# Kernel tuning notes

Hardware: AMD Instinct MI355X
Metric: run time of the kernel (lower is better)

The kernel has to match this reference:

```python
import jax, jax.numpy as jnp
import numpy as np

FEATURE_DIM = 128
HIDDEN_DIM = 64
MAPPING_SIZE = 64
SCALE = 10.0
B, N, H, W = 8, 65536, 56, 56


def setup_inputs() -> dict:
    key = jax.random.key(0)
    ks = jax.random.split(key, 12)
    features = jax.random.normal(ks[0], (B, FEATURE_DIM, H, W), dtype=jnp.float32)
    # points in [-1, 1]^3
    points = jax.random.uniform(ks[1], (B, N, 3), dtype=jnp.float32, minval=-1.0, maxval=1.0)
    # realistic pinhole intrinsics for a 56x56 feature map
    k_mat = jnp.array([[56.0, 0.0, 28.0], [0.0, 56.0, 28.0], [0.0, 0.0, 1.0]], dtype=jnp.float32)
    k = jnp.broadcast_to(k_mat, (B, 3, 3))
    # extrinsics: identity rotation, translate z by 2 so points are in front of camera
    rt_mat = jnp.concatenate([jnp.eye(3, dtype=jnp.float32), jnp.array([[0.0], [0.0], [2.0]], dtype=jnp.float32)], axis=1)
    rt = jnp.broadcast_to(rt_mat, (B, 3, 4))
    # learned params
    B_gauss = jax.random.normal(ks[2], (MAPPING_SIZE, 3), dtype=jnp.float32) * SCALE
    input_dim = FEATURE_DIM + 2 * MAPPING_SIZE
    W1 = jax.random.normal(ks[3], (input_dim, HIDDEN_DIM), dtype=jnp.float32) * 0.05
    b1 = jnp.zeros((HIDDEN_DIM,), dtype=jnp.float32)
    W2 = jax.random.normal(ks[4], (HIDDEN_DIM, HIDDEN_DIM), dtype=jnp.float32) * 0.05
    b2 = jnp.zeros((HIDDEN_DIM,), dtype=jnp.float32)
    W3 = jax.random.normal(ks[5], (HIDDEN_DIM, HIDDEN_DIM), dtype=jnp.float32) * 0.05
    b3 = jnp.zeros((HIDDEN_DIM,), dtype=jnp.float32)
    W4 = jax.random.normal(ks[6], (HIDDEN_DIM, 1), dtype=jnp.float32) * 0.05
    b4 = jnp.zeros((1,), dtype=jnp.float32)
    return {"features": features, "points": points, "k": k, "rt": rt,
            "B_gauss": B_gauss, "W1": W1, "b1": b1, "W2": W2, "b2": b2,
            "W3": W3, "b3": b3, "W4": W4, "b4": b4}


def _grid_sample_bilinear_zeros(grid, x, y):
    # grid: (B, C, H, W); x, y: (B, N) pixel coords (align_corners=False already unnormalized)
    Bc, C, Hc, Wc = grid.shape
    g = jnp.transpose(grid, (0, 2, 3, 1))  # (B, H, W, C)
    x0 = jnp.floor(x)
    y0 = jnp.floor(y)
    wx1 = x - x0  # frac
    wy1 = y - y0
    wx0 = 1.0 - wx1
    wy0 = 1.0 - wy1
    x0i = x0.astype(jnp.int32)
    y0i = y0.astype(jnp.int32)
    bidx = jnp.arange(Bc, dtype=jnp.int32)[:, None]  # (B, 1)

    def gather(ix, iy):
        inb = ((ix >= 0) & (ix < Wc) & (iy >= 0) & (iy < Hc)).astype(grid.dtype)  # (B, N)
        vals = g[bidx, jnp.clip(iy, 0, Hc - 1), jnp.clip(ix, 0, Wc - 1)]  # (B, N, C)
        return vals * inb[..., None]

    out = (gather(x0i, y0i) * (wx0 * wy0)[..., None]
           + gather(x0i + 1, y0i) * (wx1 * wy0)[..., None]
           + gather(x0i, y0i + 1) * (wx0 * wy1)[..., None]
           + gather(x0i + 1, y0i + 1) * (wx1 * wy1)[..., None])
    return out  # (B, N, C)


def reference(features, points, k, rt, B_gauss, W1, b1, W2, b2, W3, b3, W4, b4):
    Bc, Nc, _ = points.shape
    Hc, Wc = features.shape[-2:]
    # --- camera projection ---
    homo = jnp.concatenate([points, jnp.ones((Bc, Nc, 1), dtype=points.dtype)], axis=2)  # (B,N,4)
    cam = jnp.einsum('bij,bnj->bni', rt, homo)   # (B,N,3)
    img = jnp.einsum('bij,bnj->bni', k, cam)     # (B,N,3)
    z = img[:, :, 2:3] + 1e-8
    uv = img[:, :, :2] / z
    valid = (img[:, :, 2:3] > 0).astype(points.dtype)  # (B,N,1)
    u_norm = (2.0 * uv[..., 0] + 1.0) / Wc - 1.0
    v_norm = (2.0 * uv[..., 1] + 1.0) / Hc - 1.0
    # grid_sample align_corners=False unnormalization: ix = ((g+1)*W - 1)/2
    x = ((u_norm + 1.0) * Wc - 1.0) * 0.5
    y = ((v_norm + 1.0) * Hc - 1.0) * 0.5
    img_feats = _grid_sample_bilinear_zeros(features, x, y) * valid  # (B,N,C)
    # --- Fourier mapping ---
    x_proj = (2.0 * np.pi) * jnp.einsum('bnd,md->bnm', points, B_gauss)  # (B,N,M)
    coord_feats = jnp.concatenate([jnp.sin(x_proj), jnp.cos(x_proj)], axis=-1)  # (B,N,2M)
    # --- MLP ---
    inp = jnp.concatenate([img_feats, coord_feats], axis=2)  # (B,N,C+2M)
    h = jax.nn.relu(inp @ W1 + b1)
    h = jax.nn.relu(h @ W2 + b2)
    h = jax.nn.relu(h @ W3 + b3)
    out = h @ W4 + b4  # (B,N,1)
    return out
```

## Files before the change

kernel.cpp:

```cpp
#include <hip/hip_runtime.h>

#define FDIM 128
#define HDIM 64
#define MSIZE 64
#define IMG_W 56
#define IMG_H 56
#define NPIX (IMG_W * IMG_H)
#define NB 8
#define NPTS 65536

typedef _Float16 f16x8 __attribute__((ext_vector_type(8)));
typedef __fp16 hf16x2 __attribute__((ext_vector_type(2)));
typedef float f32x4 __attribute__((ext_vector_type(4)));
typedef int i32x4 __attribute__((ext_vector_type(4)));

#define W2_OFF 16384
#define W3_OFF 20480
#define FT_BYTE_OFF 49152
#define TR16_BLOCKS (NPIX / 16 * NB)

__device__ __forceinline__ void lds_fence() {
    __asm__ volatile("s_waitcnt lgkmcnt(0)" ::: "memory");
}

__global__ __launch_bounds__(256) void prep_kernel(const float* __restrict__ in,
                                                   const float* __restrict__ W1,
                                                   const float* __restrict__ W2,
                                                   const float* __restrict__ W3,
                                                   _Float16* __restrict__ ws) {
    if (blockIdx.x < TR16_BLOCKS) {
        __shared__ float tile[16][133];
        _Float16* out = ws + FT_BYTE_OFF / 2;
        const int b = blockIdx.x / (NPIX / 16);
        const int pbase = (blockIdx.x % (NPIX / 16)) * 16;
        const int t = threadIdx.x;
        const float* src = in + (size_t)b * FDIM * NPIX;
        _Float16*    dst = out + (size_t)b * NPIX * FDIM;
        const int pq = t & 3;
        const int ch = t >> 2;
#pragma unroll
        for (int it = 0; it < 2; ++it) {
            const int c = it * 64 + ch;
            const float4 v = *(const float4*)(src + (size_t)c * NPIX + pbase + pq * 4);
            tile[pq * 4 + 0][c] = v.x;
            tile[pq * 4 + 1][c] = v.y;
            tile[pq * 4 + 2][c] = v.z;
            tile[pq * 4 + 3][c] = v.w;
        }
        __syncthreads();
        const int px = t >> 4;
        const int hk = (t & 15) * 8;
        union { f16x8 v; hf16x2 h[4]; } hv;
#pragma unroll
        for (int j = 0; j < 4; ++j)
            hv.h[j] = __builtin_amdgcn_cvt_pkrtz(tile[px][hk + 2 * j], tile[px][hk + 2 * j + 1]);
        *(f16x8*)(dst + (size_t)(pbase + px) * FDIM + hk) = hv.v;
    } else {
        const int t = (blockIdx.x - TR16_BLOCKS) * 256 + threadIdx.x;
        const int l = t & 63;
        const int q = l >> 4;
        const int col = l & 15;
        const int frag = t >> 6;
        if (frag < 32) {
            const int kt = frag >> 2, nt = frag & 3;
#pragma unroll
            for (int j = 0; j < 8; ++j) {
                int k = kt * 32 + q * 8 + j;
                int row = (k < 128) ? k : (128 + (k & 1) * 64 + ((k - 128) >> 1));
                ws[((size_t)(frag * 64 + l)) * 8 + j] = (_Float16)W1[row * HDIM + nt * 16 + col];
            }
        } else if (frag < 40) {
            const int f2 = frag - 32;
            const int kt = f2 >> 2, nt = f2 & 3;
#pragma unroll
            for (int j = 0; j < 8; ++j) {
                int row = kt * 32 + q * 8 + j;
                ws[W2_OFF + ((size_t)(f2 * 64 + l)) * 8 + j] = (_Float16)W2[row * HDIM + nt * 16 + col];
            }
        } else {
            const int f3 = frag - 40;
            const int kt = f3 >> 2, nt = f3 & 3;
#pragma unroll
            for (int j = 0; j < 8; ++j) {
                int row = kt * 32 + q * 8 + j;
                ws[W3_OFF + ((size_t)(f3 * 64 + l)) * 8 + j] = (_Float16)W3[row * HDIM + nt * 16 + col];
            }
        }
    }
}

__global__ __launch_bounds__(256, 4) void decoder_mfma3(
    const _Float16* __restrict__ ft,
    const float* __restrict__ points,
    const float* __restrict__ Kmat, const float* __restrict__ Rt,
    const float* __restrict__ Bg,
    const _Float16* __restrict__ wfrag,
    const float* __restrict__ b1, const float* __restrict__ b2,
    const float* __restrict__ b3,
    const float* __restrict__ W4, const float* __restrict__ b4,
    float* __restrict__ out) {
    __shared__ _Float16 lds[4 * 32 * 72];
    const int tid = threadIdx.x;
    const int wid = tid >> 6;
    const int l   = tid & 63;
    const int q   = l >> 4;
    const int col = l & 15;
    const int b    = blockIdx.x & 7;
    const int grp  = blockIdx.x >> 3;
    const int base = b * NPTS + grp * 128 + wid * 32;
    _Float16* Ah = lds + wid * 32 * 72;
    float* sh = (float*)Ah;
    int*   shi = (int*)Ah;

    if (l < 32) {
        const int gid = base + l;
        const float px = points[(size_t)gid * 3 + 0];
        const float py = points[(size_t)gid * 3 + 1];
        const float pz = points[(size_t)gid * 3 + 2];
        const float* rt = Rt + b * 12;
        const float* km = Kmat + b * 9;
        float cx = rt[0] * px + rt[1] * py + rt[2]  * pz + rt[3];
        float cy = rt[4] * px + rt[5] * py + rt[6]  * pz + rt[7];
        float cz = rt[8] * px + rt[9] * py + rt[10] * pz + rt[11];
        float ix = km[0] * cx + km[1] * cy + km[2] * cz;
        float iy = km[3] * cx + km[4] * cy + km[5] * cz;
        float iz = km[6] * cx + km[7] * cy + km[8] * cz;
        float z  = iz + 1e-8f;
        float u  = ix / z;
        float v  = iy / z;
        float valid = (iz > 0.0f) ? 1.0f : 0.0f;
        float u_norm = (2.0f * u + 1.0f) / (float)IMG_W - 1.0f;
        float v_norm = (2.0f * v + 1.0f) / (float)IMG_H - 1.0f;
        float x = ((u_norm + 1.0f) * (float)IMG_W - 1.0f) * 0.5f;
        float y = ((v_norm + 1.0f) * (float)IMG_H - 1.0f) * 0.5f;
        float x0f = floorf(x), y0f = floorf(y);
        float wx1 = x - x0f, wy1 = y - y0f;
        float wx0 = 1.0f - wx1, wy0 = 1.0f - wy1;
        int x0 = (int)x0f, y0 = (int)y0f;
        int x1 = x0 + 1, y1 = y0 + 1;
        int x0c = x0 < 0 ? 0 : (x0 > IMG_W - 1 ? IMG_W - 1 : x0);
        int x1c = x1 < 0 ? 0 : (x1 > IMG_W - 1 ? IMG_W - 1 : x1);
        int y0c = y0 < 0 ? 0 : (y0 > IMG_H - 1 ? IMG_H - 1 : y0);
        int y1c = y1 < 0 ? 0 : (y1 > IMG_H - 1 ? IMG_H - 1 : y1);
        float mx0 = (x0 >= 0 && x0 < IMG_W) ? 1.0f : 0.0f;
        float mx1 = (x1 >= 0 && x1 < IMG_W) ? 1.0f : 0.0f;
        float my0 = (y0 >= 0 && y0 < IMG_H) ? 1.0f : 0.0f;
        float my1 = (y1 >= 0 && y1 < IMG_H) ? 1.0f : 0.0f;
        const int pb = b * NPIX;
        sh[l * 12 + 0] = wx0 * wy0 * mx0 * my0 * valid;
        sh[l * 12 + 1] = wx1 * wy0 * mx1 * my0 * valid;
        sh[l * 12 + 2] = wx0 * wy1 * mx0 * my1 * valid;
        sh[l * 12 + 3] = wx1 * wy1 * mx1 * my1 * valid;
        shi[l * 12 + 4] = (pb + y0c * IMG_W + x0c) * FDIM;
        shi[l * 12 + 5] = (pb + y0c * IMG_W + x1c) * FDIM;
        shi[l * 12 + 6] = (pb + y1c * IMG_W + x0c) * FDIM;
        shi[l * 12 + 7] = (pb + y1c * IMG_W + x1c) * FDIM;
        sh[l * 12 + 8]  = px;
        sh[l * 12 + 9]  = py;
        sh[l * 12 + 10] = pz;
    }
    lds_fence();

    const f32x4 zero4 = {0.0f, 0.0f, 0.0f, 0.0f};
    f32x4 acc[2][4];
#pragma unroll
    for (int mt = 0; mt < 2; ++mt)
#pragma unroll
        for (int nt = 0; nt < 4; ++nt) acc[mt][nt] = zero4;

    f32x4 wv[2];
    i32x4 iv[2];
    float qx[2], qy[2], qz[2];
#pragma unroll
    for (int mt = 0; mt < 2; ++mt) {
        const float* e = sh + (mt * 16 + col) * 12;
        wv[mt] = *(const f32x4*)(e);
        iv[mt] = *(const i32x4*)(e + 4);
        qx[mt] = e[8]; qy[mt] = e[9]; qz[mt] = e[10];
    }

    f16x8 c00 = *(const f16x8*)(ft + iv[0].x + q * 8);
    f16x8 c10 = *(const f16x8*)(ft + iv[0].y + q * 8);
    f16x8 c01 = *(const f16x8*)(ft + iv[0].z + q * 8);
    f16x8 c11 = *(const f16x8*)(ft + iv[0].w + q * 8);

#pragma unroll
    for (int ktf = 0; ktf < 4; ++ktf) {
        float bgx[4], bgy[4], bgz[4];
#pragma unroll
        for (int i = 0; i < 4; ++i) {
            const int m = ktf * 16 + q * 4 + i;
            bgx[i] = Bg[m * 3 + 0];
            bgy[i] = Bg[m * 3 + 1];
            bgz[i] = Bg[m * 3 + 2];
        }
        f16x8 bf[4];
#pragma unroll
        for (int nt = 0; nt < 4; ++nt)
            bf[nt] = *(const f16x8*)(wfrag + ((size_t)(((4 + ktf) * 4 + nt) * 64 + l)) * 8);
#pragma unroll
        for (int mt = 0; mt < 2; ++mt) {
            union { f16x8 v; hf16x2 h[4]; } af;
#pragma unroll
            for (int i = 0; i < 4; ++i) {
                float t = bgx[i] * qx[mt] + bgy[i] * qy[mt] + bgz[i] * qz[mt];
                float tf = __builtin_amdgcn_fractf(t);
                af.h[i] = __builtin_amdgcn_cvt_pkrtz(__builtin_amdgcn_sinf(tf),
                                                     __builtin_amdgcn_cosf(tf));
            }
#pragma unroll
            for (int nt = 0; nt < 4; ++nt)
                acc[mt][nt] = __builtin_amdgcn_mfma_f32_16x16x32_f16(af.v, bf[nt], acc[mt][nt], 0, 0, 0);
        }
    }

    _Float16 wh[2][4];
#pragma unroll
    for (int mt = 0; mt < 2; ++mt) {
        wh[mt][0] = (_Float16)wv[mt].x; wh[mt][1] = (_Float16)wv[mt].y;
        wh[mt][2] = (_Float16)wv[mt].z; wh[mt][3] = (_Float16)wv[mt].w;
    }
#pragma unroll
    for (int s = 0; s < 8; ++s) {
        const int mt = s >> 2, ktg = s & 3;
        f16x8 n00, n10, n01, n11;
        if (s < 7) {
            const int nmt = (s + 1) >> 2, nktg = (s + 1) & 3;
            const int co = nktg * 32 + q * 8;
            n00 = *(const f16x8*)(ft + iv[nmt].x + co);
            n10 = *(const f16x8*)(ft + iv[nmt].y + co);
            n01 = *(const f16x8*)(ft + iv[nmt].z + co);
            n11 = *(const f16x8*)(ft + iv[nmt].w + co);
        }
        f16x8 af = c00 * wh[mt][0] + c10 * wh[mt][1] + c01 * wh[mt][2] + c11 * wh[mt][3];
#pragma unroll
        for (int nt = 0; nt < 4; ++nt) {
            f16x8 bf = *(const f16x8*)(wfrag + ((size_t)((ktg * 4 + nt) * 64 + l)) * 8);
            acc[mt][nt] = __builtin_amdgcn_mfma_f32_16x16x32_f16(af, bf, acc[mt][nt], 0, 0, 0);
        }
        c00 = n00; c10 = n10; c01 = n01; c11 = n11;
    }

    float bb[4];
#pragma unroll
    for (int nt = 0; nt < 4; ++nt) bb[nt] = b1[nt * 16 + col];
#pragma unroll
    for (int mt = 0; mt < 2; ++mt)
#pragma unroll
        for (int nt = 0; nt < 4; ++nt)
#pragma unroll
            for (int r = 0; r < 4; ++r) {
                float hv = fmaxf(acc[mt][nt][r] + bb[nt], 0.0f);
                Ah[(mt * 16 + q * 4 + r) * 72 + nt * 16 + col] = (_Float16)hv;
            }
    lds_fence();

#pragma unroll
    for (int mt = 0; mt < 2; ++mt)
#pragma unroll
        for (int nt = 0; nt < 4; ++nt) acc[mt][nt] = zero4;
#pragma unroll
    for (int ktl = 0; ktl < 2; ++ktl) {
        f16x8 bf[4];
#pragma unroll
        for (int nt = 0; nt < 4; ++nt)
            bf[nt] = *(const f16x8*)(wfrag + W2_OFF + ((size_t)((ktl * 4 + nt) * 64 + l)) * 8);
#pragma unroll
        for (int mt = 0; mt < 2; ++mt) {
            f16x8 af = *(const f16x8*)(&Ah[(mt * 16 + col) * 72 + ktl * 32 + q * 8]);
#pragma unroll
            for (int nt = 0; nt < 4; ++nt)
                acc[mt][nt] = __builtin_amdgcn_mfma_f32_16x16x32_f16(af, bf[nt], acc[mt][nt], 0, 0, 0);
        }
    }
    lds_fence();
#pragma unroll
    for (int nt = 0; nt < 4; ++nt) bb[nt] = b2[nt * 16 + col];
#pragma unroll
    for (int mt = 0; mt < 2; ++mt)
#pragma unroll
        for (int nt = 0; nt < 4; ++nt)
#pragma unroll
            for (int r = 0; r < 4; ++r) {
                float hv = fmaxf(acc[mt][nt][r] + bb[nt], 0.0f);
                Ah[(mt * 16 + q * 4 + r) * 72 + nt * 16 + col] = (_Float16)hv;
            }
    lds_fence();

#pragma unroll
    for (int mt = 0; mt < 2; ++mt)
#pragma unroll
        for (int nt = 0; nt < 4; ++nt) acc[mt][nt] = zero4;
#pragma unroll
    for (int ktl = 0; ktl < 2; ++ktl) {
        f16x8 bf[4];
#pragma unroll
        for (int nt = 0; nt < 4; ++nt)
            bf[nt] = *(const f16x8*)(wfrag + W3_OFF + ((size_t)((ktl * 4 + nt) * 64 + l)) * 8);
#pragma unroll
        for (int mt = 0; mt < 2; ++mt) {
            f16x8 af = *(const f16x8*)(&Ah[(mt * 16 + col) * 72 + ktl * 32 + q * 8]);
#pragma unroll
            for (int nt = 0; nt < 4; ++nt)
                acc[mt][nt] = __builtin_amdgcn_mfma_f32_16x16x32_f16(af, bf[nt], acc[mt][nt], 0, 0, 0);
        }
    }

    float b3v[4], w4v[4];
#pragma unroll
    for (int nt = 0; nt < 4; ++nt) {
        b3v[nt] = b3[nt * 16 + col];
        w4v[nt] = W4[nt * 16 + col];
    }
    const float b4v = b4[0];
#pragma unroll
    for (int mt = 0; mt < 2; ++mt)
#pragma unroll
        for (int r = 0; r < 4; ++r) {
            float p = 0.0f;
#pragma unroll
            for (int nt = 0; nt < 4; ++nt)
                p = fmaf(fmaxf(acc[mt][nt][r] + b3v[nt], 0.0f), w4v[nt], p);
            p += __shfl_xor(p, 1);
            p += __shfl_xor(p, 2);
            p += __shfl_xor(p, 4);
            p += __shfl_xor(p, 8);
            if (col == 0) out[base + mt * 16 + q * 4 + r] = p + b4v;
        }
}

__global__ __launch_bounds__(64, 2) void decoder_valu(
    const float* __restrict__ feats, const float* __restrict__ points,
    const float* __restrict__ Kmat, const float* __restrict__ Rt,
    const float* __restrict__ Bg,
    const float* __restrict__ W1, const float* __restrict__ b1,
    const float* __restrict__ W2, const float* __restrict__ b2,
    const float* __restrict__ W3, const float* __restrict__ b3,
    const float* __restrict__ W4, const float* __restrict__ b4,
    float* __restrict__ out) {
    __shared__ float hbuf[64 * 65];
    const int tid = threadIdx.x;
    const int b   = blockIdx.x / (NPTS / 64);
    const int gid = blockIdx.x * 64 + tid;
    const float px = points[(size_t)gid * 3 + 0];
    const float py = points[(size_t)gid * 3 + 1];
    const float pz = points[(size_t)gid * 3 + 2];
    const float* rt = Rt + b * 12;
    const float* km = Kmat + b * 9;
    float cx = rt[0] * px + rt[1] * py + rt[2]  * pz + rt[3];
    float cy = rt[4] * px + rt[5] * py + rt[6]  * pz + rt[7];
    float cz = rt[8] * px + rt[9] * py + rt[10] * pz + rt[11];
    float ix = km[0] * cx + km[1] * cy + km[2] * cz;
    float iy = km[3] * cx + km[4] * cy + km[5] * cz;
    float iz = km[6] * cx + km[7] * cy + km[8] * cz;
    float z  = iz + 1e-8f;
    float u  = ix / z, v = iy / z;
    float valid = (iz > 0.0f) ? 1.0f : 0.0f;
    float u_norm = (2.0f * u + 1.0f) / (float)IMG_W - 1.0f;
    float v_norm = (2.0f * v + 1.0f) / (float)IMG_H - 1.0f;
    float x = ((u_norm + 1.0f) * (float)IMG_W - 1.0f) * 0.5f;
    float y = ((v_norm + 1.0f) * (float)IMG_H - 1.0f) * 0.5f;
    float x0f = floorf(x), y0f = floorf(y);
    float wx1 = x - x0f, wy1 = y - y0f;
    float wx0 = 1.0f - wx1, wy0 = 1.0f - wy1;
    int x0 = (int)x0f, y0 = (int)y0f;
    int x1 = x0 + 1, y1 = y0 + 1;
    int x0c = x0 < 0 ? 0 : (x0 > IMG_W - 1 ? IMG_W - 1 : x0);
    int x1c = x1 < 0 ? 0 : (x1 > IMG_W - 1 ? IMG_W - 1 : x1);
    int y0c = y0 < 0 ? 0 : (y0 > IMG_H - 1 ? IMG_H - 1 : y0);
    int y1c = y1 < 0 ? 0 : (y1 > IMG_H - 1 ? IMG_H - 1 : y1);
    float mx0 = (x0 >= 0 && x0 < IMG_W) ? 1.0f : 0.0f;
    float mx1 = (x1 >= 0 && x1 < IMG_W) ? 1.0f : 0.0f;
    float my0 = (y0 >= 0 && y0 < IMG_H) ? 1.0f : 0.0f;
    float my1 = (y1 >= 0 && y1 < IMG_H) ? 1.0f : 0.0f;
    float w00 = wx0 * wy0 * mx0 * my0 * valid;
    float w10 = wx1 * wy0 * mx1 * my0 * valid;
    float w01 = wx0 * wy1 * mx0 * my1 * valid;
    float w11 = wx1 * wy1 * mx1 * my1 * valid;
    float h[HDIM];
#pragma unroll
    for (int j = 0; j < HDIM; ++j) h[j] = b1[j];
    const float* fb = feats + (size_t)b * FDIM * NPIX;
    const int p00 = y0c * IMG_W + x0c, p10 = y0c * IMG_W + x1c;
    const int p01 = y1c * IMG_W + x0c, p11 = y1c * IMG_W + x1c;
#pragma unroll 1
    for (int c = 0; c < FDIM; ++c) {
        const float* fp = fb + (size_t)c * NPIX;
        float fv = w00 * fp[p00] + w10 * fp[p10] + w01 * fp[p01] + w11 * fp[p11];
        const float* wr = W1 + (size_t)c * HDIM;
#pragma unroll
        for (int j = 0; j < HDIM; ++j) h[j] = fmaf(fv, wr[j], h[j]);
    }
#pragma unroll 1
    for (int m = 0; m < MSIZE; ++m) {
        float t = Bg[m * 3 + 0] * px + Bg[m * 3 + 1] * py + Bg[m * 3 + 2] * pz;
        float tf = t - floorf(t);
        float s = __builtin_amdgcn_sinf(tf);
        float c = __builtin_amdgcn_cosf(tf);
        const float* wsn = W1 + (size_t)(FDIM + m) * HDIM;
        const float* wcs = W1 + (size_t)(FDIM + MSIZE + m) * HDIM;
#pragma unroll
        for (int j = 0; j < HDIM; ++j)
            h[j] = fmaf(s, wsn[j], fmaf(c, wcs[j], h[j]));
    }
    float* myh = &hbuf[tid * 65];
#pragma unroll
    for (int j = 0; j < HDIM; ++j) myh[j] = fmaxf(h[j], 0.0f);
    float h2[HDIM];
#pragma unroll
    for (int j = 0; j < HDIM; ++j) h2[j] = b2[j];
#pragma unroll 1
    for (int i = 0; i < HDIM; ++i) {
        float hi = myh[i];
        const float* wr = W2 + (size_t)i * HDIM;
#pragma unroll
        for (int j = 0; j < HDIM; ++j) h2[j] = fmaf(hi, wr[j], h2[j]);
    }
#pragma unroll
    for (int j = 0; j < HDIM; ++j) myh[j] = fmaxf(h2[j], 0.0f);
#pragma unroll
    for (int j = 0; j < HDIM; ++j) h[j] = b3[j];
#pragma unroll 1
    for (int i = 0; i < HDIM; ++i) {
        float hi = myh[i];
        const float* wr = W3 + (size_t)i * HDIM;
#pragma unroll
        for (int j = 0; j < HDIM; ++j) h[j] = fmaf(hi, wr[j], h[j]);
    }
    float acc = b4[0];
#pragma unroll
    for (int j = 0; j < HDIM; ++j) acc = fmaf(fmaxf(h[j], 0.0f), W4[j], acc);
    out[gid] = acc;
}

extern "C" void kernel_launch(void* const* d_in, const int* in_sizes, int n_in,
                              void* d_out, int out_size, void* d_ws, size_t ws_size,
                              hipStream_t stream) {
    const float* feats = (const float*)d_in[0];
    const float* pts   = (const float*)d_in[1];
    const float* k     = (const float*)d_in[2];
    const float* rt    = (const float*)d_in[3];
    const float* Bg    = (const float*)d_in[4];
    const float* W1    = (const float*)d_in[5];
    const float* b1    = (const float*)d_in[6];
    const float* W2    = (const float*)d_in[7];
    const float* b2    = (const float*)d_in[8];
    const float* W3    = (const float*)d_in[9];
    const float* b3    = (const float*)d_in[10];
    const float* W4    = (const float*)d_in[11];
    const float* b4    = (const float*)d_in[12];
    float* out = (float*)d_out;

    const size_t ftBytes = (size_t)NB * NPIX * FDIM * sizeof(_Float16);

    if (ws_size >= FT_BYTE_OFF + ftBytes) {
        _Float16* wf = (_Float16*)d_ws;
        _Float16* ft = (_Float16*)((char*)d_ws + FT_BYTE_OFF);
        prep_kernel<<<TR16_BLOCKS + 12, 256, 0, stream>>>(feats, W1, W2, W3, wf);
        decoder_mfma3<<<NB * NPTS / 128, 256, 0, stream>>>(ft, pts, k, rt, Bg, wf,
                                                           b1, b2, b3, W4, b4, out);
    } else {
        decoder_valu<<<NB * NPTS / 64, 64, 0, stream>>>(feats, pts, k, rt, Bg,
                                                        W1, b1, W2, b2, W3, b3, W4, b4, out);
    }
}
```

Baseline: 182.3 us.

## Shuffle per-point data in registers and deepen gather prefetch pipeline

Per-point projection results are now computed redundantly by all 64 lanes and distributed with wave shuffles, replacing the LDS staging round trip and fence. The bilinear feature gather prefetch goes from one to two steps ahead, the W2/W3 weight fragments are loaded before the LDS activation write so their latency overlaps it, and the occupancy hint drops from 4 to 3 blocks per CU. This raises register pressure and may reduce occupancy in exchange for more latency hiding on the random gathers.

```diff
diff --git a/kernel.cpp b/kernel.cpp
--- a/kernel.cpp
+++ b/kernel.cpp
@@ -12,7 +12,6 @@
 typedef _Float16 f16x8 __attribute__((ext_vector_type(8)));
 typedef __fp16 hf16x2 __attribute__((ext_vector_type(2)));
 typedef float f32x4 __attribute__((ext_vector_type(4)));
-typedef int i32x4 __attribute__((ext_vector_type(4)));
 
 #define W2_OFF 16384
 #define W3_OFF 20480
@@ -89,7 +88,7 @@
     }
 }
 
-__global__ __launch_bounds__(256, 4) void decoder_mfma3(
+__global__ __launch_bounds__(256, 3) void decoder_mfma4(
     const _Float16* __restrict__ ft,
     const float* __restrict__ points,
     const float* __restrict__ Kmat, const float* __restrict__ Rt,
@@ -109,11 +108,9 @@
     const int grp  = blockIdx.x >> 3;
     const int base = b * NPTS + grp * 128 + wid * 32;
     _Float16* Ah = lds + wid * 32 * 72;
-    float* sh = (float*)Ah;
-    int*   shi = (int*)Ah;
-
-    if (l < 32) {
-        const int gid = base + l;
+
+    {
+        const int gid = base + (l & 31);
         const float px = points[(size_t)gid * 3 + 0];
         const float py = points[(size_t)gid * 3 + 1];
         const float pz = points[(size_t)gid * 3 + 2];
@@ -147,186 +144,198 @@
         float my0 = (y0 >= 0 && y0 < IMG_H) ? 1.0f : 0.0f;
         float my1 = (y1 >= 0 && y1 < IMG_H) ? 1.0f : 0.0f;
         const int pb = b * NPIX;
-        sh[l * 12 + 0] = wx0 * wy0 * mx0 * my0 * valid;
-        sh[l * 12 + 1] = wx1 * wy0 * mx1 * my0 * valid;
-        sh[l * 12 + 2] = wx0 * wy1 * mx0 * my1 * valid;
-        sh[l * 12 + 3] = wx1 * wy1 * mx1 * my1 * valid;
-        shi[l * 12 + 4] = (pb + y0c * IMG_W + x0c) * FDIM;
-        shi[l * 12 + 5] = (pb + y0c * IMG_W + x1c) * FDIM;
-        shi[l * 12 + 6] = (pb + y1c * IMG_W + x0c) * FDIM;
-        shi[l * 12 + 7] = (pb + y1c * IMG_W + x1c) * FDIM;
-        sh[l * 12 + 8]  = px;
-        sh[l * 12 + 9]  = py;
-        sh[l * 12 + 10] = pz;
-    }
-    lds_fence();
-
-    const f32x4 zero4 = {0.0f, 0.0f, 0.0f, 0.0f};
-    f32x4 acc[2][4];
-#pragma unroll
-    for (int mt = 0; mt < 2; ++mt)
-#pragma unroll
-        for (int nt = 0; nt < 4; ++nt) acc[mt][nt] = zero4;
-
-    f32x4 wv[2];
-    i32x4 iv[2];
-    float qx[2], qy[2], qz[2];
-#pragma unroll
-    for (int mt = 0; mt < 2; ++mt) {
-        const float* e = sh + (mt * 16 + col) * 12;
-        wv[mt] = *(const f32x4*)(e);
-        iv[mt] = *(const i32x4*)(e + 4);
-        qx[mt] = e[8]; qy[mt] = e[9]; qz[mt] = e[10];
-    }
-
-    f16x8 c00 = *(const f16x8*)(ft + iv[0].x + q * 8);
-    f16x8 c10 = *(const f16x8*)(ft + iv[0].y + q * 8);
-    f16x8 c01 = *(const f16x8*)(ft + iv[0].z + q * 8);
-    f16x8 c11 = *(const f16x8*)(ft + iv[0].w + q * 8);
-
-#pragma unroll
-    for (int ktf = 0; ktf < 4; ++ktf) {
-        float bgx[4], bgy[4], bgz[4];
-#pragma unroll
-        for (int i = 0; i < 4; ++i) {
-            const int m = ktf * 16 + q * 4 + i;
-            bgx[i] = Bg[m * 3 + 0];
-            bgy[i] = Bg[m * 3 + 1];
-            bgz[i] = Bg[m * 3 + 2];
-        }
-        f16x8 bf[4];
-#pragma unroll
-        for (int nt = 0; nt < 4; ++nt)
-            bf[nt] = *(const f16x8*)(wfrag + ((size_t)(((4 + ktf) * 4 + nt) * 64 + l)) * 8);
+        float r_w00 = wx0 * wy0 * mx0 * my0 * valid;
+        float r_w10 = wx1 * wy0 * mx1 * my0 * valid;
+        float r_w01 = wx0 * wy1 * mx0 * my1 * valid;
+        float r_w11 = wx1 * wy1 * mx1 * my1 * valid;
+        int r_i00 = (pb + y0c * IMG_W + x0c) * FDIM;
+        int r_i10 = (pb + y0c * IMG_W + x1c) * FDIM;
+        int r_i01 = (pb + y1c * IMG_W + x0c) * FDIM;
+        int r_i11 = (pb + y1c * IMG_W + x1c) * FDIM;
+
+        float wv0[2], wv1[2], wv2[2], wv3[2];
+        int   iv0[2], iv1[2], iv2[2], iv3[2];
+        float qx[2], qy[2], qz[2];
 #pragma unroll
         for (int mt = 0; mt < 2; ++mt) {
-            union { f16x8 v; hf16x2 h[4]; } af;
+            const int src = mt * 16 + col;
+            wv0[mt] = __shfl(r_w00, src);
+            wv1[mt] = __shfl(r_w10, src);
+            wv2[mt] = __shfl(r_w01, src);
+            wv3[mt] = __shfl(r_w11, src);
+            iv0[mt] = __shfl(r_i00, src);
+            iv1[mt] = __shfl(r_i10, src);
+            iv2[mt] = __shfl(r_i01, src);
+            iv3[mt] = __shfl(r_i11, src);
+            qx[mt]  = __shfl(px, src);
+            qy[mt]  = __shfl(py, src);
+            qz[mt]  = __shfl(pz, src);
+        }
+
+        const f32x4 zero4 = {0.0f, 0.0f, 0.0f, 0.0f};
+        f32x4 acc[2][4];
+#pragma unroll
+        for (int mt = 0; mt < 2; ++mt)
+#pragma unroll
+            for (int nt = 0; nt < 4; ++nt) acc[mt][nt] = zero4;
+
+        const int co0 = q * 8;
+        f16x8 a00 = *(const f16x8*)(ft + iv0[0] + co0);
+        f16x8 a10 = *(const f16x8*)(ft + iv1[0] + co0);
+        f16x8 a01 = *(const f16x8*)(ft + iv2[0] + co0);
+        f16x8 a11 = *(const f16x8*)(ft + iv3[0] + co0);
+        const int co1 = 32 + q * 8;
+        f16x8 e00 = *(const f16x8*)(ft + iv0[0] + co1);
+        f16x8 e10 = *(const f16x8*)(ft + iv1[0] + co1);
+        f16x8 e01 = *(const f16x8*)(ft + iv2[0] + co1);
+        f16x8 e11 = *(const f16x8*)(ft + iv3[0] + co1);
+
+#pragma unroll
+        for (int ktf = 0; ktf < 4; ++ktf) {
+            float bgx[4], bgy[4], bgz[4];
 #pragma unroll
             for (int i = 0; i < 4; ++i) {
-                float t = bgx[i] * qx[mt] + bgy[i] * qy[mt] + bgz[i] * qz[mt];
-                float tf = __builtin_amdgcn_fractf(t);
-                af.h[i] = __builtin_amdgcn_cvt_pkrtz(__builtin_amdgcn_sinf(tf),
-                                                     __builtin_amdgcn_cosf(tf));
-            }
+                const int m = ktf * 16 + q * 4 + i;
+                bgx[i] = Bg[m * 3 + 0];
+                bgy[i] = Bg[m * 3 + 1];
+                bgz[i] = Bg[m * 3 + 2];
+            }
+            f16x8 bf[4];
 #pragma unroll
             for (int nt = 0; nt < 4; ++nt)
-                acc[mt][nt] = __builtin_amdgcn_mfma_f32_16x16x32_f16(af.v, bf[nt], acc[mt][nt], 0, 0, 0);
-        }
-    }
-
-    _Float16 wh[2][4];
-#pragma unroll
-    for (int mt = 0; mt < 2; ++mt) {
-        wh[mt][0] = (_Float16)wv[mt].x; wh[mt][1] = (_Float16)wv[mt].y;
-        wh[mt][2] = (_Float16)wv[mt].z; wh[mt][3] = (_Float16)wv[mt].w;
-    }
-#pragma unroll
-    for (int s = 0; s < 8; ++s) {
-        const int mt = s >> 2, ktg = s & 3;
-        f16x8 n00, n10, n01, n11;
-        if (s < 7) {
-            const int nmt = (s + 1) >> 2, nktg = (s + 1) & 3;
-            const int co = nktg * 32 + q * 8;
-            n00 = *(const f16x8*)(ft + iv[nmt].x + co);
-            n10 = *(const f16x8*)(ft + iv[nmt].y + co);
-            n01 = *(const f16x8*)(ft + iv[nmt].z + co);
-            n11 = *(const f16x8*)(ft + iv[nmt].w + co);
-        }
-        f16x8 af = c00 * wh[mt][0] + c10 * wh[mt][1] + c01 * wh[mt][2] + c11 * wh[mt][3];
+                bf[nt] = *(const f16x8*)(wfrag + ((size_t)(((4 + ktf) * 4 + nt) * 64 + l)) * 8);
+#pragma unroll
+            for (int mt = 0; mt < 2; ++mt) {
+                union { f16x8 v; hf16x2 h[4]; } af;
+#pragma unroll
+                for (int i = 0; i < 4; ++i) {
+                    float t = bgx[i] * qx[mt] + bgy[i] * qy[mt] + bgz[i] * qz[mt];
+                    float tf = __builtin_amdgcn_fractf(t);
+                    af.h[i] = __builtin_amdgcn_cvt_pkrtz(__builtin_amdgcn_sinf(tf),
+                                                         __builtin_amdgcn_cosf(tf));
+                }
+#pragma unroll
+                for (int nt = 0; nt < 4; ++nt)
+                    acc[mt][nt] = __builtin_amdgcn_mfma_f32_16x16x32_f16(af.v, bf[nt], acc[mt][nt], 0, 0, 0);
+            }
+        }
+
+        _Float16 wh[2][4];
+#pragma unroll
+        for (int mt = 0; mt < 2; ++mt) {
+            wh[mt][0] = (_Float16)wv0[mt]; wh[mt][1] = (_Float16)wv1[mt];
+            wh[mt][2] = (_Float16)wv2[mt]; wh[mt][3] = (_Float16)wv3[mt];
+        }
+#pragma unroll
+        for (int s = 0; s < 8; ++s) {
+            const int mt = s >> 2;
+            f16x8 t00, t10, t01, t11;
+            if (s < 6) {
+                const int nmt = (s + 2) >> 2, nktg = (s + 2) & 3;
+                const int co = nktg * 32 + q * 8;
+                t00 = *(const f16x8*)(ft + iv0[nmt] + co);
+                t10 = *(const f16x8*)(ft + iv1[nmt] + co);
+                t01 = *(const f16x8*)(ft + iv2[nmt] + co);
+                t11 = *(const f16x8*)(ft + iv3[nmt] + co);
+            }
+            f16x8 af = a00 * wh[mt][0] + a10 * wh[mt][1] + a01 * wh[mt][2] + a11 * wh[mt][3];
+            const int ktg = s & 3;
+#pragma unroll
+            for (int nt = 0; nt < 4; ++nt) {
+                f16x8 bf = *(const f16x8*)(wfrag + ((size_t)((ktg * 4 + nt) * 64 + l)) * 8);
+                acc[mt][nt] = __builtin_amdgcn_mfma_f32_16x16x32_f16(af, bf, acc[mt][nt], 0, 0, 0);
+            }
+            a00 = e00; a10 = e10; a01 = e01; a11 = e11;
+            e00 = t00; e10 = t10; e01 = t01; e11 = t11;
+        }
+
+        f16x8 bfW[8];
+#pragma unroll
+        for (int f = 0; f < 8; ++f)
+            bfW[f] = *(const f16x8*)(wfrag + W2_OFF + ((size_t)(f * 64 + l)) * 8);
+
+        float bb[4];
+#pragma unroll
+        for (int nt = 0; nt < 4; ++nt) bb[nt] = b1[nt * 16 + col];
+#pragma unroll
+        for (int mt = 0; mt < 2; ++mt)
+#pragma unroll
+            for (int nt = 0; nt < 4; ++nt)
+#pragma unroll
+                for (int r = 0; r < 4; ++r) {
+                    float hv = fmaxf(acc[mt][nt][r] + bb[nt], 0.0f);
+                    Ah[(mt * 16 + q * 4 + r) * 72 + nt * 16 + col] = (_Float16)hv;
+                }
+        lds_fence();
+
+#pragma unroll
+        for (int mt = 0; mt < 2; ++mt)
+#pragma unroll
+            for (int nt = 0; nt < 4; ++nt) acc[mt][nt] = zero4;
+#pragma unroll
+        for (int ktl = 0; ktl < 2; ++ktl)
+#pragma unroll
+            for (int mt = 0; mt < 2; ++mt) {
+                f16x8 af = *(const f16x8*)(&Ah[(mt * 16 + col) * 72 + ktl * 32 + q * 8]);
+#pragma unroll
+                for (int nt = 0; nt < 4; ++nt)
+                    acc[mt][nt] = __builtin_amdgcn_mfma_f32_16x16x32_f16(af, bfW[ktl * 4 + nt], acc[mt][nt], 0, 0, 0);
+            }
+
+#pragma unroll
+        for (int f = 0; f < 8; ++f)
+            bfW[f] = *(const f16x8*)(wfrag + W3_OFF + ((size_t)(f * 64 + l)) * 8);
+
+        lds_fence();
+#pragma unroll
+        for (int nt = 0; nt < 4; ++nt) bb[nt] = b2[nt * 16 + col];
+#pragma unroll
+        for (int mt = 0; mt < 2; ++mt)
+#pragma unroll
+            for (int nt = 0; nt < 4; ++nt)
+#pragma unroll
+                for (int r = 0; r < 4; ++r) {
+                    float hv = fmaxf(acc[mt][nt][r] + bb[nt], 0.0f);
+                    Ah[(mt * 16 + q * 4 + r) * 72 + nt * 16 + col] = (_Float16)hv;
+                }
+        lds_fence();
+
+#pragma unroll
+        for (int mt = 0; mt < 2; ++mt)
+#pragma unroll
+            for (int nt = 0; nt < 4; ++nt) acc[mt][nt] = zero4;
+#pragma unroll
+        for (int ktl = 0; ktl < 2; ++ktl)
+#pragma unroll
+            for (int mt = 0; mt < 2; ++mt) {
+                f16x8 af = *(const f16x8*)(&Ah[(mt * 16 + col) * 72 + ktl * 32 + q * 8]);
+#pragma unroll
+                for (int nt = 0; nt < 4; ++nt)
+                    acc[mt][nt] = __builtin_amdgcn_mfma_f32_16x16x32_f16(af, bfW[ktl * 4 + nt], acc[mt][nt], 0, 0, 0);
+            }
+
+        float b3v[4], w4v[4];
 #pragma unroll
         for (int nt = 0; nt < 4; ++nt) {
-            f16x8 bf = *(const f16x8*)(wfrag + ((size_t)((ktg * 4 + nt) * 64 + l)) * 8);
-            acc[mt][nt] = __builtin_amdgcn_mfma_f32_16x16x32_f16(af, bf, acc[mt][nt], 0, 0, 0);
-        }
-        c00 = n00; c10 = n10; c01 = n01; c11 = n11;
-    }
-
-    float bb[4];
-#pragma unroll
-    for (int nt = 0; nt < 4; ++nt) bb[nt] = b1[nt * 16 + col];
-#pragma unroll
-    for (int mt = 0; mt < 2; ++mt)
-#pragma unroll
-        for (int nt = 0; nt < 4; ++nt)
+            b3v[nt] = b3[nt * 16 + col];
+            w4v[nt] = W4[nt * 16 + col];
+        }
+        const float b4v = b4[0];
+#pragma unroll
+        for (int mt = 0; mt < 2; ++mt)
 #pragma unroll
             for (int r = 0; r < 4; ++r) {
-                float hv = fmaxf(acc[mt][nt][r] + bb[nt], 0.0f);
-                Ah[(mt * 16 + q * 4 + r) * 72 + nt * 16 + col] = (_Float16)hv;
-            }
-    lds_fence();
-
-#pragma unroll
-    for (int mt = 0; mt < 2; ++mt)
-#pragma unroll
-        for (int nt = 0; nt < 4; ++nt) acc[mt][nt] = zero4;
-#pragma unroll
-    for (int ktl = 0; ktl < 2; ++ktl) {
-        f16x8 bf[4];
-#pragma unroll
-        for (int nt = 0; nt < 4; ++nt)
-            bf[nt] = *(const f16x8*)(wfrag + W2_OFF + ((size_t)((ktl * 4 + nt) * 64 + l)) * 8);
-#pragma unroll
-        for (int mt = 0; mt < 2; ++mt) {
-            f16x8 af = *(const f16x8*)(&Ah[(mt * 16 + col) * 72 + ktl * 32 + q * 8]);
-#pragma unroll
-            for (int nt = 0; nt < 4; ++nt)
-                acc[mt][nt] = __builtin_amdgcn_mfma_f32_16x16x32_f16(af, bf[nt], acc[mt][nt], 0, 0, 0);
-        }
-    }
-    lds_fence();
-#pragma unroll
-    for (int nt = 0; nt < 4; ++nt) bb[nt] = b2[nt * 16 + col];
-#pragma unroll
-    for (int mt = 0; mt < 2; ++mt)
-#pragma unroll
-        for (int nt = 0; nt < 4; ++nt)
-#pragma unroll
-            for (int r = 0; r < 4; ++r) {
-                float hv = fmaxf(acc[mt][nt][r] + bb[nt], 0.0f);
-                Ah[(mt * 16 + q * 4 + r) * 72 + nt * 16 + col] = (_Float16)hv;
-            }
-    lds_fence();
-
-#pragma unroll
-    for (int mt = 0; mt < 2; ++mt)
-#pragma unroll
-        for (int nt = 0; nt < 4; ++nt) acc[mt][nt] = zero4;
-#pragma unroll
-    for (int ktl = 0; ktl < 2; ++ktl) {
-        f16x8 bf[4];
-#pragma unroll
-        for (int nt = 0; nt < 4; ++nt)
-            bf[nt] = *(const f16x8*)(wfrag + W3_OFF + ((size_t)((ktl * 4 + nt) * 64 + l)) * 8);
-#pragma unroll
-        for (int mt = 0; mt < 2; ++mt) {
-            f16x8 af = *(const f16x8*)(&Ah[(mt * 16 + col) * 72 + ktl * 32 + q * 8]);
-#pragma unroll
-            for (int nt = 0; nt < 4; ++nt)
-                acc[mt][nt] = __builtin_amdgcn_mfma_f32_16x16x32_f16(af, bf[nt], acc[mt][nt], 0, 0, 0);
-        }
-    }
-
-    float b3v[4], w4v[4];
-#pragma unroll
-    for (int nt = 0; nt < 4; ++nt) {
-        b3v[nt] = b3[nt * 16 + col];
-        w4v[nt] = W4[nt * 16 + col];
-    }
-    const float b4v = b4[0];
-#pragma unroll
-    for (int mt = 0; mt < 2; ++mt)
-#pragma unroll
-        for (int r = 0; r < 4; ++r) {
-            float p = 0.0f;
-#pragma unroll
-            for (int nt = 0; nt < 4; ++nt)
-                p = fmaf(fmaxf(acc[mt][nt][r] + b3v[nt], 0.0f), w4v[nt], p);
-            p += __shfl_xor(p, 1);
-            p += __shfl_xor(p, 2);
-            p += __shfl_xor(p, 4);
-            p += __shfl_xor(p, 8);
-            if (col == 0) out[base + mt * 16 + q * 4 + r] = p + b4v;
-        }
+                float p = 0.0f;
+#pragma unroll
+                for (int nt = 0; nt < 4; ++nt)
+                    p = fmaf(fmaxf(acc[mt][nt][r] + b3v[nt], 0.0f), w4v[nt], p);
+                p += __shfl_xor(p, 1);
+                p += __shfl_xor(p, 2);
+                p += __shfl_xor(p, 4);
+                p += __shfl_xor(p, 8);
+                if (col == 0) out[base + mt * 16 + q * 4 + r] = p + b4v;
+            }
+    }
 }
 
 __global__ __launch_bounds__(64, 2) void decoder_valu(
@@ -457,7 +466,7 @@
         _Float16* wf = (_Float16*)d_ws;
         _Float16* ft = (_Float16*)((char*)d_ws + FT_BYTE_OFF);
         prep_kernel<<<TR16_BLOCKS + 12, 256, 0, stream>>>(feats, W1, W2, W3, wf);
-        decoder_mfma3<<<NB * NPTS / 128, 256, 0, stream>>>(ft, pts, k, rt, Bg, wf,
+        decoder_mfma4<<<NB * NPTS / 128, 256, 0, stream>>>(ft, pts, k, rt, Bg, wf,
                                                            b1, b2, b3, W4, b4, out);
     } else {
         decoder_valu<<<NB * NPTS / 64, 64, 0, stream>>>(feats, pts, k, rt, Bg,
```

Result: no change. 184.0 us (+0.9%).
